# Optimization experiments

Measured on AMD Instinct MI355X. Metric: run time of the kernel, lower is better.

## Reference

```python
import jax, jax.numpy as jnp
import numpy as np
from jax.scipy.special import gammaln

RES = 512    # init res
STEPS = 128  # init steps


def setup_inputs() -> dict:
    key = jax.random.key(0)
    # control points in [0,1]^2: [batch, n_strks, n_points, 2]
    control_points = jax.random.uniform(key, (16, 4, 4, 2), dtype=jnp.float32)
    sigma = jnp.float32(0.02)  # Gaussian kernel bandwidth
    return {"control_points": control_points, "sigma": sigma}


def _bernstein(order, n_steps):
    # feat[k, t] = C(order, k) * t**(order-k) * (1-t)**k, matching sample_curve
    t = jnp.linspace(0.0, 1.0, n_steps, dtype=jnp.float32)          # [T]
    k = jnp.arange(order + 1, dtype=jnp.float32)[:, None]           # [K,1]
    o = jnp.float32(order)
    log_comb = gammaln(o + 1.0) - gammaln(k + 1.0) - gammaln(o - k + 1.0)
    return jnp.exp(log_comb) * t[None, :] ** (o - k) * (1.0 - t[None, :]) ** k  # [K,T]


def reference(control_points, sigma):
    """Bezier.forward with method='base', keep_strk_dim=True.
    Returns [batch, n_strks, 1, res, res]."""
    b, s, n_pts, _ = control_points.shape
    feat = _bernstein(n_pts - 1, STEPS)                              # [K,T]
    curve = jnp.einsum('bcki,kt->bcit', control_points, feat)       # [b,s,2,T]
    x = curve[:, :, 0]                                               # [b,s,T]
    y = curve[:, :, 1]                                               # [b,s,T]
    g = jnp.arange(RES, dtype=jnp.float32) / RES                     # pixel coords
    inv = 1.0 / (2.0 * sigma ** 2)
    # Gaussian splat is separable: exp(-(dx^2+dy^2)/2s^2) = exp(-dx^2/2s^2)*exp(-dy^2/2s^2)
    # raster[b,s,p,q] = sum_t Ay[b,s,t,p] * Ax[b,s,t,q]  (x indexes columns q, y rows p,
    # matching torch meshgrid + transpose(1,3) layout)
    Ax = jnp.exp(-(x[..., None] - g) ** 2 * inv)                     # [b,s,T,res]
    Ay = jnp.exp(-(y[..., None] - g) ** 2 * inv)                     # [b,s,T,res]
    raster = jnp.einsum('bstp,bstq->bspq', Ay, Ax)                   # [b,s,res,res]
    return raster[:, :, None]                                        # [b,s,1,res,res]
```

## Files before the change

### kernel.cpp

```cpp
#include <hip/hip_runtime.h>
#include <math.h>

#define RES   512
#define STEPS 128
#define TILE  64
#define CHUNK 32

__global__ __launch_bounds__(256) void bezier_raster_kernel(
    const float* __restrict__ cp,
    const float* __restrict__ sigma_ptr,
    float* __restrict__ out)
{
    __shared__ float xs[STEPS];
    __shared__ float ys[STEPS];
    __shared__ int   tlist[STEPS];
    __shared__ int   nact_s;
    __shared__ float axs[CHUNK][TILE];
    __shared__ float ays[CHUNK][TILE];

    const int img = blockIdx.z;
    const int q0  = blockIdx.x * TILE;
    const int p0  = blockIdx.y * TILE;
    const int tid = threadIdx.x;

    const float sigma  = sigma_ptr[0];
    const float inv    = 1.0f / (2.0f * sigma * sigma);
    const float margin = sqrtf(23.0f / inv);

    if (tid == 0) nact_s = 0;
    __syncthreads();

    if (tid < STEPS) {
        const float w  = (float)tid * (1.0f / (float)(STEPS - 1));
        const float v  = 1.0f - w;
        const float b0 = w * w * w;
        const float b1 = 3.0f * w * w * v;
        const float b2 = 3.0f * w * v * v;
        const float b3 = v * v * v;
        const float* c = cp + (size_t)img * 8;
        const float x = c[0]*b0 + c[2]*b1 + c[4]*b2 + c[6]*b3;
        const float y = c[1]*b0 + c[3]*b1 + c[5]*b2 + c[7]*b3;
        xs[tid] = x;
        ys[tid] = y;
        const float gqlo = (float)q0 * (1.0f / RES) - margin;
        const float gqhi = (float)(q0 + TILE - 1) * (1.0f / RES) + margin;
        const float gplo = (float)p0 * (1.0f / RES) - margin;
        const float gphi = (float)(p0 + TILE - 1) * (1.0f / RES) + margin;
        if (x >= gqlo && x <= gqhi && y >= gplo && y <= gphi) {
            int slot = atomicAdd(&nact_s, 1);
            tlist[slot] = tid;
        }
    }
    __syncthreads();
    const int nact = nact_s;

    float acc[4][4];
    #pragma unroll
    for (int i = 0; i < 4; ++i)
        #pragma unroll
        for (int j = 0; j < 4; ++j) acc[i][j] = 0.0f;

    const int ty = tid >> 4;
    const int tx = tid & 15;

    for (int base = 0; base < nact; base += CHUNK) {
        const int cnt  = min(CHUNK, nact - base);
        const int cntp = (cnt + 3) & ~3;
        for (int e = tid; e < cntp * TILE; e += 256) {
            const int r   = e >> 6;
            const int col = e & (TILE - 1);
            if (r < cnt) {
                const int   t  = tlist[base + r];
                const float gq = (float)(q0 + col) * (1.0f / RES);
                const float gp = (float)(p0 + col) * (1.0f / RES);
                const float dx = xs[t] - gq;
                const float dy = ys[t] - gp;
                axs[r][col] = __expf(-(dx * dx) * inv);
                ays[r][col] = __expf(-(dy * dy) * inv);
            } else {
                axs[r][col] = 0.0f;
                ays[r][col] = 0.0f;
            }
        }
        __syncthreads();
        for (int r = 0; r < cntp; r += 4) {
            #pragma unroll
            for (int rr = 0; rr < 4; ++rr) {
                const float4 av = *(const float4*)&ays[r + rr][ty * 4];
                const float4 bv = *(const float4*)&axs[r + rr][tx * 4];
                acc[0][0] += av.x * bv.x; acc[0][1] += av.x * bv.y;
                acc[0][2] += av.x * bv.z; acc[0][3] += av.x * bv.w;
                acc[1][0] += av.y * bv.x; acc[1][1] += av.y * bv.y;
                acc[1][2] += av.y * bv.z; acc[1][3] += av.y * bv.w;
                acc[2][0] += av.z * bv.x; acc[2][1] += av.z * bv.y;
                acc[2][2] += av.z * bv.z; acc[2][3] += av.z * bv.w;
                acc[3][0] += av.w * bv.x; acc[3][1] += av.w * bv.y;
                acc[3][2] += av.w * bv.z; acc[3][3] += av.w * bv.w;
            }
        }
        __syncthreads();
    }

    #pragma unroll
    for (int i = 0; i < 4; ++i) {
        const int p = p0 + ty * 4 + i;
        float4 v;
        v.x = acc[i][0]; v.y = acc[i][1]; v.z = acc[i][2]; v.w = acc[i][3];
        *(float4*)&out[((size_t)img * RES + p) * RES + q0 + tx * 4] = v;
    }
}

extern "C" void kernel_launch(void* const* d_in, const int* in_sizes, int n_in,
                              void* d_out, int out_size, void* d_ws, size_t ws_size,
                              hipStream_t stream) {
    const float* cp    = (const float*)d_in[0];
    const float* sigma = (const float*)d_in[1];
    float* out         = (float*)d_out;
    const int n_img    = in_sizes[0] / 8;
    dim3 grid(RES / TILE, RES / TILE, n_img);
    bezier_raster_kernel<<<grid, 256, 0, stream>>>(cp, sigma, out);
}
```

Measured before the change: 94.53 us.

## Restructure raster into full-width row strips with per-step wavefront culling

Each block now covers an 8-row by 512-column strip of one image instead of a 64x64 tile. Curve steps are culled once by the y-band, and the per-row Gaussian weights are precomputed in shared memory. Each thread owns two columns and skips steps when the whole wavefront is outside the x-margin. This drops the chunked shared-memory GEMM and its barriers in favour of per-thread exp plus FMA with warp-level skipping. The culling margin is tightened from 23 to 16 sigma-squared units, which may add small truncation error.

Measured after the change: 97.30 us. 2.9% more time.

```diff
diff --git a/kernel.cpp b/kernel.cpp
--- a/kernel.cpp
+++ b/kernel.cpp
@@ -3,35 +3,32 @@
 
 #define RES   512
 #define STEPS 128
-#define TILE  64
-#define CHUNK 32
+#define BH    8
 
-__global__ __launch_bounds__(256) void bezier_raster_kernel(
+__global__ __launch_bounds__(256) void bezier_rows_kernel(
     const float* __restrict__ cp,
     const float* __restrict__ sigma_ptr,
     float* __restrict__ out)
 {
-    __shared__ float xs[STEPS];
-    __shared__ float ys[STEPS];
-    __shared__ int   tlist[STEPS];
+    __shared__ float xc[STEPS];
+    __shared__ float yc[STEPS];
+    __shared__ float ayc[STEPS][BH];
     __shared__ int   nact_s;
-    __shared__ float axs[CHUNK][TILE];
-    __shared__ float ays[CHUNK][TILE];
 
-    const int img = blockIdx.z;
-    const int q0  = blockIdx.x * TILE;
-    const int p0  = blockIdx.y * TILE;
+    const int img = blockIdx.y;
+    const int p0  = blockIdx.x * BH;
     const int tid = threadIdx.x;
 
-    const float sigma  = sigma_ptr[0];
-    const float inv    = 1.0f / (2.0f * sigma * sigma);
-    const float margin = sqrtf(23.0f / inv);
+    const float sigma = sigma_ptr[0];
+    const float inv   = 1.0f / (2.0f * sigma * sigma);
+    const float msq   = 16.0f / inv;
+    const float margin = sqrtf(msq);
 
     if (tid == 0) nact_s = 0;
     __syncthreads();
 
     if (tid < STEPS) {
-        const float w  = (float)tid * (1.0f / (float)(STEPS - 1));
+        const float w  = (float)tid * (1.0f / 127.0f);
         const float v  = 1.0f - w;
         const float b0 = w * w * w;
         const float b1 = 3.0f * w * w * v;
@@ -40,73 +37,60 @@
         const float* c = cp + (size_t)img * 8;
         const float x = c[0]*b0 + c[2]*b1 + c[4]*b2 + c[6]*b3;
         const float y = c[1]*b0 + c[3]*b1 + c[5]*b2 + c[7]*b3;
-        xs[tid] = x;
-        ys[tid] = y;
-        const float gqlo = (float)q0 * (1.0f / RES) - margin;
-        const float gqhi = (float)(q0 + TILE - 1) * (1.0f / RES) + margin;
-        const float gplo = (float)p0 * (1.0f / RES) - margin;
-        const float gphi = (float)(p0 + TILE - 1) * (1.0f / RES) + margin;
-        if (x >= gqlo && x <= gqhi && y >= gplo && y <= gphi) {
-            int slot = atomicAdd(&nact_s, 1);
-            tlist[slot] = tid;
+        const float lo = (float)p0          * (1.0f / RES) - margin;
+        const float hi = (float)(p0 + BH-1) * (1.0f / RES) + margin;
+        if (y >= lo && y <= hi) {
+            const int s = atomicAdd(&nact_s, 1);
+            xc[s] = x;
+            yc[s] = y;
         }
     }
     __syncthreads();
     const int nact = nact_s;
 
-    float acc[4][4];
-    #pragma unroll
-    for (int i = 0; i < 4; ++i)
-        #pragma unroll
-        for (int j = 0; j < 4; ++j) acc[i][j] = 0.0f;
+    for (int e = tid; e < nact * BH; e += 256) {
+        const int s = e >> 3;
+        const int i = e & (BH - 1);
+        const float dy = yc[s] - (float)(p0 + i) * (1.0f / RES);
+        ayc[s][i] = __expf(-dy * dy * inv);
+    }
+    __syncthreads();
 
-    const int ty = tid >> 4;
-    const int tx = tid & 15;
+    float acc0[BH] = {0.f,0.f,0.f,0.f,0.f,0.f,0.f,0.f};
+    float acc1[BH] = {0.f,0.f,0.f,0.f,0.f,0.f,0.f,0.f};
+    const float gq0 = (float)tid         * (1.0f / RES);
+    const float gq1 = (float)(tid + 256) * (1.0f / RES);
 
-    for (int base = 0; base < nact; base += CHUNK) {
-        const int cnt  = min(CHUNK, nact - base);
-        const int cntp = (cnt + 3) & ~3;
-        for (int e = tid; e < cntp * TILE; e += 256) {
-            const int r   = e >> 6;
-            const int col = e & (TILE - 1);
-            if (r < cnt) {
-                const int   t  = tlist[base + r];
-                const float gq = (float)(q0 + col) * (1.0f / RES);
-                const float gp = (float)(p0 + col) * (1.0f / RES);
-                const float dx = xs[t] - gq;
-                const float dy = ys[t] - gp;
-                axs[r][col] = __expf(-(dx * dx) * inv);
-                ays[r][col] = __expf(-(dy * dy) * inv);
-            } else {
-                axs[r][col] = 0.0f;
-                ays[r][col] = 0.0f;
-            }
+    for (int s = 0; s < nact; ++s) {
+        const float xv  = xc[s];
+        const float dx0 = xv - gq0;
+        const float dx1 = xv - gq1;
+        const int h0 = __any(dx0 * dx0 < msq);
+        const int h1 = __any(dx1 * dx1 < msq);
+        if (!(h0 | h1)) continue;
+        const float4 a0 = *(const float4*)&ayc[s][0];
+        const float4 a1 = *(const float4*)&ayc[s][4];
+        if (h0) {
+            const float ax = __expf(-dx0 * dx0 * inv);
+            acc0[0] += ax * a0.x; acc0[1] += ax * a0.y;
+            acc0[2] += ax * a0.z; acc0[3] += ax * a0.w;
+            acc0[4] += ax * a1.x; acc0[5] += ax * a1.y;
+            acc0[6] += ax * a1.z; acc0[7] += ax * a1.w;
         }
-        __syncthreads();
-        for (int r = 0; r < cntp; r += 4) {
-            #pragma unroll
-            for (int rr = 0; rr < 4; ++rr) {
-                const float4 av = *(const float4*)&ays[r + rr][ty * 4];
-                const float4 bv = *(const float4*)&axs[r + rr][tx * 4];
-                acc[0][0] += av.x * bv.x; acc[0][1] += av.x * bv.y;
-                acc[0][2] += av.x * bv.z; acc[0][3] += av.x * bv.w;
-                acc[1][0] += av.y * bv.x; acc[1][1] += av.y * bv.y;
-                acc[1][2] += av.y * bv.z; acc[1][3] += av.y * bv.w;
-                acc[2][0] += av.z * bv.x; acc[2][1] += av.z * bv.y;
-                acc[2][2] += av.z * bv.z; acc[2][3] += av.z * bv.w;
-                acc[3][0] += av.w * bv.x; acc[3][1] += av.w * bv.y;
-                acc[3][2] += av.w * bv.z; acc[3][3] += av.w * bv.w;
-            }
+        if (h1) {
+            const float ax = __expf(-dx1 * dx1 * inv);
+            acc1[0] += ax * a0.x; acc1[1] += ax * a0.y;
+            acc1[2] += ax * a0.z; acc1[3] += ax * a0.w;
+            acc1[4] += ax * a1.x; acc1[5] += ax * a1.y;
+            acc1[6] += ax * a1.z; acc1[7] += ax * a1.w;
         }
-        __syncthreads();
     }
 
     #pragma unroll
-    for (int i = 0; i < 4; ++i) {
-        const int p = p0 + ty * 4 + i;
-        float4 v;
-        v.x = acc[i][0]; v.y = acc[i][1]; v.z = acc[i][2]; v.w = acc[i][3];
-        *(float4*)&out[((size_t)img * RES + p) * RES + q0 + tx * 4] = v;
+    for (int i = 0; i < BH; ++i) {
+        const size_t rowoff = ((size_t)img * RES + (size_t)(p0 + i)) * RES;
+        out[rowoff + tid]       = acc0[i];
+        out[rowoff + tid + 256] = acc1[i];
     }
 }
 
@@ -117,6 +101,6 @@
     const float* sigma = (const float*)d_in[1];
     float* out         = (float*)d_out;
     const int n_img    = in_sizes[0] / 8;
-    dim3 grid(RES / TILE, RES / TILE, n_img);
-    bezier_raster_kernel<<<grid, 256, 0, stream>>>(cp, sigma, out);
+    dim3 grid(RES / BH, n_img);
+    bezier_rows_kernel<<<grid, 256, 0, stream>>>(cp, sigma, out);
 }
```
